# Kernel optimization log

Measured on AMD Instinct MI355X. Metric: run time of the kernel, lower is better.

The kernel has to match this reference:

```python
import jax, jax.numpy as jnp
import numpy as np

N = 2048   # graph nodes
K = 3      # Chebyshev order of LSTM cell graph conv
IN = 2     # input feature dim (in/out flow)
H = 64     # hidden dim
B = 16     # batch
T = 12     # encoder sequence length


def _cheb(L, x, order):
    """Chebyshev polynomial features. x: [B, N, F] -> [B, N, order*F]."""
    Tk = [x]
    if order > 1:
        Tk.append(jnp.einsum('nm,bmf->bnf', L, x))
    for _ in range(2, order):
        Tk.append(2.0 * jnp.einsum('nm,bmf->bnf', L, Tk[-1]) - Tk[-2])
    return jnp.concatenate(Tk, axis=-1)


def _cell(L, x, h, c, W, b):
    """Graph-conv LSTM cell. x: [B,N,IN], h/c: [B,N,H]."""
    comb = jnp.concatenate([x, h], axis=-1)          # [B, N, IN+H]
    gates = _cheb(L, comb, K) @ W + b                # [B, N, 4H]
    i, f, o, g = jnp.split(gates, 4, axis=-1)
    c2 = jax.nn.sigmoid(f) * c + jax.nn.sigmoid(i) * jnp.tanh(g)
    h2 = jax.nn.sigmoid(o) * jnp.tanh(c2)
    return h2, c2


def setup_inputs() -> dict:
    rng = np.random.default_rng(0)
    # random sparse symmetric adjacency (avg degree ~8) -> normalized Laplacian
    A = rng.random((N, N)) < 8.0 / N
    A = np.triu(A, 1)
    A = (A | A.T).astype(np.float32)
    d = np.clip(A.sum(1), 1.0, None)
    dinv = 1.0 / np.sqrt(d)
    Lap = (np.eye(N, dtype=np.float32) - dinv[:, None] * A * dinv[None, :]).astype(np.float32)

    key = jax.random.key(0)
    k1, k2, k3 = jax.random.split(key, 3)
    return {
        'input_tensor': jax.random.normal(k1, (B, T, N, IN), jnp.float32),
        'L': jnp.asarray(Lap),
        'W_cell': jax.random.normal(k2, (K * (IN + H), 4 * H), jnp.float32) * 0.05,
        'b_cell': jnp.zeros((4 * H,), jnp.float32),
        'W0': jax.random.normal(k3, (H, IN), jnp.float32) * 0.05,
        'b0': jnp.zeros((IN,), jnp.float32),
        'future': 12,
    }


def reference(input_tensor, L, W_cell, b_cell, W0, b0, future):
    bsz = input_tensor.shape[0]
    h0 = jnp.zeros((bsz, N, H), input_tensor.dtype)
    c0 = jnp.zeros((bsz, N, H), input_tensor.dtype)

    # encoder: unroll ConvLSTM over the input sequence
    def enc_step(carry, xt):
        h, c = carry
        h, c = _cell(L, xt, h, c, W_cell, b_cell)
        return (h, c), None

    (h, c), _ = jax.lax.scan(enc_step, (h0, c0), jnp.swapaxes(input_tensor, 0, 1))

    # conv0 has K=1 => per-node linear; first prediction from last hidden state
    x = jnp.tanh(h @ W0 + b0)                         # [B, N, IN]

    def dec_step(carry, _):
        h, c, x = carry
        h, c = _cell(L, x, h, c, W_cell, b_cell)
        x2 = jnp.tanh(h @ W0 + b0)
        return (h, c, x2), x2

    _, xs = jax.lax.scan(dec_step, (h, c, x), None, length=future - 1)
    if future > 1:
        out = jnp.concatenate([x[:, None], jnp.swapaxes(xs, 0, 1)], axis=1)
    else:
        out = x[:, None]
    return out  # [B, future, N, IN]
```

## Files before the change

### kernel.cpp

```cpp
#include <hip/hip_runtime.h>
#include <cstdint>
#include <cstddef>

#define NN   2048
#define BB   16
#define TT   12
#define FUT  12
#define HH   64
#define GG   256
#define KP   224
#define ELLW 72
#define ASTR 232

typedef __attribute__((ext_vector_type(8))) short bf16x8;
typedef __attribute__((ext_vector_type(4))) float f32x4;

__device__ __forceinline__ float sigmoidf_(float x) {
    return 1.f / (1.f + __expf(-x));
}
__device__ __forceinline__ float tanhf_(float x) {
    const float e = __expf(2.f * x);
    return 1.f - 2.f / (e + 1.f);
}
__device__ __forceinline__ unsigned short f2bf(float x) {
    unsigned u = __builtin_bit_cast(unsigned, x);
    u += 0x7fffu + ((u >> 16) & 1u);
    return (unsigned short)(u >> 16);
}
__device__ __forceinline__ float bf2f(unsigned short s) {
    unsigned u = ((unsigned)s) << 16;
    return __builtin_bit_cast(float, u);
}

__global__ __launch_bounds__(256) void build_ell(
    const float* __restrict__ L, int* __restrict__ cols,
    float* __restrict__ vals, int* __restrict__ cnt)
{
    const int n = blockIdx.x;
    const int t = threadIdx.x;
    const float* row = L + (size_t)n * NN;
    float v[8];
    int c = 0;
#pragma unroll
    for (int i = 0; i < 8; ++i) {
        v[i] = row[t * 8 + i];
        c += (v[i] != 0.f);
    }
    __shared__ int s[256];
    s[t] = c;
    __syncthreads();
    for (int d = 1; d < 256; d <<= 1) {
        int add = (t >= d) ? s[t - d] : 0;
        __syncthreads();
        s[t] += add;
        __syncthreads();
    }
    int o = s[t] - c;
#pragma unroll
    for (int i = 0; i < 8; ++i) {
        if (v[i] != 0.f) {
            if (o < ELLW) {
                cols[n * ELLW + o] = t * 8 + i;
                vals[n * ELLW + o] = v[i];
            }
            ++o;
        }
    }
    if (t == 255) {
        int cn = (s[255] < ELLW) ? s[255] : ELLW;
        int cn4 = (cn + 3) & ~3;
        if (cn4 > ELLW) cn4 = ELLW;
        for (int p = cn; p < cn4; ++p) {
            cols[n * ELLW + p] = n;
            vals[n * ELLW + p] = 0.f;
        }
        cnt[n] = cn4;
    }
}

__global__ __launch_bounds__(256) void wt_prep(
    const float* __restrict__ W, short* __restrict__ Wh, short* __restrict__ Wl)
{
    const int col = blockIdx.x;
    const int k = threadIdx.x;
    if (k < KP) {
        const float x = (k < 198) ? W[(size_t)k * GG + col] : 0.f;
        const unsigned short h = f2bf(x);
        const unsigned short l = f2bf(x - bf2f(h));
        Wh[(size_t)col * KP + k] = (short)h;
        Wl[(size_t)col * KP + k] = (short)l;
    }
}

__global__ __launch_bounds__(256) void x_trans(
    const float* __restrict__ input, float* __restrict__ xt)
{
    const int o = blockIdx.x * 256 + threadIdx.x;
    const int e = o & 1;
    const int b = (o >> 1) & 15;
    const int n = (o >> 5) & (NN - 1);
    const int t = o >> 16;
    xt[o] = input[(((size_t)b * TT + t) * NN + n) * 2 + e];
}

__global__ __launch_bounds__(256) void spmm_t1(
    const float* __restrict__ xt,
    const float* __restrict__ h,
    const int* __restrict__ cols, const float* __restrict__ vals,
    const int* __restrict__ cnt,
    float* __restrict__ t1h, float* __restrict__ t1x)
{
    const int w = threadIdx.x >> 6, lane = threadIdx.x & 63;
    const int b = lane >> 2, j = lane & 3;
    const int n = blockIdx.x;
    const int cn = cnt[n];
    const int* cp = cols + n * ELLW;
    const float* vp = vals + n * ELLW;
    const int qoff = (4 * w + j) * 4;
    float a0 = 0.f, a1 = 0.f, a2 = 0.f, a3 = 0.f;
    float ax0 = 0.f, ax1 = 0.f;
#pragma unroll 4
    for (int jj = 0; jj < cn; ++jj) {
        const int m = cp[jj];
        const float v = vp[jj];
        const float4 g = *(const float4*)&h[((size_t)m * 16 + b) * HH + qoff];
        a0 += v * g.x; a1 += v * g.y; a2 += v * g.z; a3 += v * g.w;
        if (w == 0) {
            const float2 xg = *(const float2*)&xt[((size_t)m * 16 + b) * 2];
            ax0 += v * xg.x; ax1 += v * xg.y;
        }
    }
    *(float4*)&t1h[((size_t)n * 16 + b) * HH + qoff] = (float4){a0, a1, a2, a3};
    if (w == 0 && j == 0) {
        t1x[((size_t)n * 16 + b) * 2]     = ax0;
        t1x[((size_t)n * 16 + b) * 2 + 1] = ax1;
    }
}

__global__ __launch_bounds__(256, 4) void cell_fused(
    const float* __restrict__ xt,
    float* __restrict__ h, float* __restrict__ c,
    const float* __restrict__ t1h,
    const float* __restrict__ t1x,
    const int* __restrict__ cols, const float* __restrict__ vals,
    const int* __restrict__ cnt,
    const short* __restrict__ Wh, const short* __restrict__ Wl,
    const float* __restrict__ bc,
    const float* __restrict__ W0, const float* __restrict__ b0,
    float* __restrict__ xout,
    float* __restrict__ out, int jslot)
{
    __shared__ unsigned short Ah[32][ASTR];
    __shared__ unsigned short Al[32][ASTR];
    __shared__ float proj[4][32][2];
    const int tid = threadIdx.x, w = tid >> 6, lane = tid & 63;
    const int q = lane >> 4, c16 = lane & 15;
    const int b = lane >> 2, j = lane & 3;
    const int n0 = blockIdx.x * 2;
    const int qoff = (4 * w + j) * 4;

    auto put = [&](int r, int k, float v) {
        const unsigned short hi = f2bf(v);
        Ah[r][k] = hi;
        Al[r][k] = f2bf(v - bf2f(hi));
    };

    {
        const int zr = tid >> 3, zs = tid & 7;
#pragma unroll
        for (int k0 = 198; k0 < 232; k0 += 8) {
            const int k = k0 + zs;
            if (k < 232) { Ah[zr][k] = 0; Al[zr][k] = 0; }
        }
    }

#pragma unroll
    for (int ln = 0; ln < 2; ++ln) {
        const int n = n0 + ln;
        const size_t rb = (size_t)n * 16 + b;
        const int r = ln * 16 + b;
        const float4 hq = *(const float4*)&h[rb * HH + qoff];
        const float4 tq = *(const float4*)&t1h[rb * HH + qoff];
        float xo0 = 0.f, xo1 = 0.f, t160 = 0.f, t161 = 0.f;
        if (w == 1) {
            const float2 xv = *(const float2*)&xt[rb * 2];
            xo0 = xv.x; xo1 = xv.y;
            const float2 tv = *(const float2*)&t1x[rb * 2];
            t160 = tv.x; t161 = tv.y;
        }
        const int cn = cnt[n];
        const int* cp = cols + n * ELLW;
        const float* vp = vals + n * ELLW;
        float a0 = 0.f, a1 = 0.f, a2 = 0.f, a3 = 0.f, ax0 = 0.f, ax1 = 0.f;
#pragma unroll 4
        for (int jj = 0; jj < cn; ++jj) {
            const int m = cp[jj];
            const float v = vp[jj];
            const size_t mb = (size_t)m * 16 + b;
            const float4 g = *(const float4*)&t1h[mb * HH + qoff];
            a0 += v * g.x; a1 += v * g.y; a2 += v * g.z; a3 += v * g.w;
            if (w == 1) {
                const float2 gx = *(const float2*)&t1x[mb * 2];
                ax0 += v * gx.x; ax1 += v * gx.y;
            }
        }
        put(r, 2 + qoff + 0, hq.x);  put(r, 2 + qoff + 1, hq.y);
        put(r, 2 + qoff + 2, hq.z);  put(r, 2 + qoff + 3, hq.w);
        put(r, 68 + qoff + 0, tq.x); put(r, 68 + qoff + 1, tq.y);
        put(r, 68 + qoff + 2, tq.z); put(r, 68 + qoff + 3, tq.w);
        put(r, 134 + qoff + 0, 2.f * a0 - hq.x);
        put(r, 134 + qoff + 1, 2.f * a1 - hq.y);
        put(r, 134 + qoff + 2, 2.f * a2 - hq.z);
        put(r, 134 + qoff + 3, 2.f * a3 - hq.w);
        if (w == 1 && j == 0) {
            put(r, 0, xo0);   put(r, 1, xo1);
            put(r, 66, t160); put(r, 67, t161);
            put(r, 132, 2.f * ax0 - xo0);
            put(r, 133, 2.f * ax1 - xo1);
        }
    }
    __syncthreads();

    f32x4 acc[2][4];
#pragma unroll
    for (int rt = 0; rt < 2; ++rt)
#pragma unroll
        for (int g = 0; g < 4; ++g) acc[rt][g] = (f32x4){0.f, 0.f, 0.f, 0.f};

    for (int kc = 0; kc < 7; ++kc) {
        const int ko = kc * 32 + q * 8;
        bf16x8 ah[2], al[2];
#pragma unroll
        for (int rt = 0; rt < 2; ++rt) {
            ah[rt] = *(const bf16x8*)&Ah[rt * 16 + c16][ko];
            al[rt] = *(const bf16x8*)&Al[rt * 16 + c16][ko];
        }
        bf16x8 bh[4], bl[4];
#pragma unroll
        for (int g = 0; g < 4; ++g) {
            const int col = (w + 4 * g) * 16 + c16;
            const size_t wo = (size_t)col * KP + ko;
            bh[g] = *(const bf16x8*)(Wh + wo);
            bl[g] = *(const bf16x8*)(Wl + wo);
        }
#pragma unroll
        for (int rt = 0; rt < 2; ++rt)
#pragma unroll
            for (int g = 0; g < 4; ++g) {
                acc[rt][g] = __builtin_amdgcn_mfma_f32_16x16x32_bf16(ah[rt], bh[g], acc[rt][g], 0, 0, 0);
                acc[rt][g] = __builtin_amdgcn_mfma_f32_16x16x32_bf16(al[rt], bh[g], acc[rt][g], 0, 0, 0);
                acc[rt][g] = __builtin_amdgcn_mfma_f32_16x16x32_bf16(ah[rt], bl[g], acc[rt][g], 0, 0, 0);
            }
    }

    const int u = 16 * w + c16;
    const float bi = bc[u], bfv = bc[64 + u], bo = bc[128 + u], bg = bc[192 + u];
    float h2v[2][4];
#pragma unroll
    for (int rt = 0; rt < 2; ++rt) {
        const int n = n0 + rt;
#pragma unroll
        for (int reg = 0; reg < 4; ++reg) {
            const int bb = q * 4 + reg;
            const size_t idx = ((size_t)n * 16 + bb) * HH + u;
            const float ig = sigmoidf_(acc[rt][0][reg] + bi);
            const float fg = sigmoidf_(acc[rt][1][reg] + bfv);
            const float og = sigmoidf_(acc[rt][2][reg] + bo);
            const float gg = tanhf_(acc[rt][3][reg] + bg);
            const float c2 = fg * c[idx] + ig * gg;
            const float h2 = og * tanhf_(c2);
            c[idx] = c2;
            h[idx] = h2;
            h2v[rt][reg] = h2;
        }
    }

    if (jslot >= 0) {
        const float w0u = W0[u * 2], w1u = W0[u * 2 + 1];
#pragma unroll
        for (int rt = 0; rt < 2; ++rt) {
#pragma unroll
            for (int reg = 0; reg < 4; ++reg) {
                float s0 = h2v[rt][reg] * w0u;
                float s1 = h2v[rt][reg] * w1u;
#pragma unroll
                for (int d = 1; d <= 8; d <<= 1) {
                    s0 += __shfl_xor(s0, d, 64);
                    s1 += __shfl_xor(s1, d, 64);
                }
                if (c16 == 0) {
                    const int lr = rt * 16 + q * 4 + reg;
                    proj[w][lr][0] = s0;
                    proj[w][lr][1] = s1;
                }
            }
        }
        __syncthreads();
        if (tid < 64) {
            const int lr = tid >> 1, comp = tid & 1;
            const float v = proj[0][lr][comp] + proj[1][lr][comp] +
                            proj[2][lr][comp] + proj[3][lr][comp] + b0[comp];
            const float y = tanhf_(v);
            const int n = n0 + (lr >> 4);
            const int bb = lr & 15;
            xout[((size_t)n * 16 + bb) * 2 + comp] = y;
            out[(((size_t)bb * FUT + jslot) * NN + n) * 2 + comp] = y;
        }
    }
}

extern "C" void kernel_launch(void* const* d_in, const int* in_sizes, int n_in,
                              void* d_out, int out_size, void* d_ws, size_t ws_size,
                              hipStream_t stream)
{
    const float* input = (const float*)d_in[0];
    const float* L     = (const float*)d_in[1];
    const float* W     = (const float*)d_in[2];
    const float* bc    = (const float*)d_in[3];
    const float* W0    = (const float*)d_in[4];
    const float* b0    = (const float*)d_in[5];

    char* ws = (char*)d_ws;
    size_t off = 0;
    auto carve = [&](size_t bytes) {
        void* p = ws + off;
        off += (bytes + 255) & ~(size_t)255;
        return p;
    };
    int*   cols  = (int*)  carve((size_t)NN * ELLW * 4);
    float* vals  = (float*)carve((size_t)NN * ELLW * 4);
    int*   cnt   = (int*)  carve((size_t)NN * 4);
    float* t1h   = (float*)carve((size_t)NN * 16 * HH * 4);
    float* t1x   = (float*)carve((size_t)NN * 16 * 2 * 4);
    float* h     = (float*)carve((size_t)NN * 16 * HH * 4);
    float* c     = (float*)carve((size_t)NN * 16 * HH * 4);
    float* xbuf  = (float*)carve((size_t)NN * 16 * 2 * 4);
    float* xtall = (float*)carve((size_t)TT * NN * 16 * 2 * 4);
    short* Wh    = (short*)carve((size_t)GG * KP * 2);
    short* Wl    = (short*)carve((size_t)GG * KP * 2);
    float* out   = (float*)d_out;

    build_ell<<<NN, 256, 0, stream>>>(L, cols, vals, cnt);
    wt_prep<<<GG, 256, 0, stream>>>(W, Wh, Wl);
    x_trans<<<(TT * NN * 16 * 2) / 256, 256, 0, stream>>>(input, xtall);
    hipMemsetAsync(h, 0, (size_t)NN * 16 * HH * 4, stream);
    hipMemsetAsync(c, 0, (size_t)NN * 16 * HH * 4, stream);

    for (int t = 0; t < TT; ++t) {
        const float* xt = xtall + (size_t)t * NN * 16 * 2;
        spmm_t1<<<NN, 256, 0, stream>>>(xt, h, cols, vals, cnt, t1h, t1x);
        cell_fused<<<NN / 2, 256, 0, stream>>>(xt, h, c, t1h, t1x, cols, vals, cnt,
                                               Wh, Wl, bc, W0, b0, xbuf, out,
                                               (t == TT - 1) ? 0 : -1);
    }
    for (int jstep = 1; jstep < FUT; ++jstep) {
        spmm_t1<<<NN, 256, 0, stream>>>(xbuf, h, cols, vals, cnt, t1h, t1x);
        cell_fused<<<NN / 2, 256, 0, stream>>>(xbuf, h, c, t1h, t1x, cols, vals, cnt,
                                               Wh, Wl, bc, W0, b0, xbuf, out, jstep);
    }
}
```

Measured before the change: 1.176 ms.

## Split second Chebyshev SpMM out of fused cell kernel into separate kernel

Moves the T2 = 2*L*T1 - T0 sparse product out of the GEMM/LSTM kernel into a new spmm_t2 kernel launched with one block per node, so the fused cell kernel only stages precomputed features. Both SpMM kernels now use a 4-wide unrolled inner loop over a count rounded up to a multiple of four, with every unused ELL slot padded with zero weights, and request higher occupancy through launch bounds. This aims to give the gather-heavy SpMM full parallelism instead of sharing blocks with the MFMA kernel. In exchange it adds an extra launch per step and extra global traffic to write and read the T2 buffers.

```diff
diff --git a/kernel.cpp b/kernel.cpp
--- a/kernel.cpp
+++ b/kernel.cpp
@@ -66,16 +66,12 @@
             ++o;
         }
     }
-    if (t == 255) {
-        int cn = (s[255] < ELLW) ? s[255] : ELLW;
-        int cn4 = (cn + 3) & ~3;
-        if (cn4 > ELLW) cn4 = ELLW;
-        for (int p = cn; p < cn4; ++p) {
-            cols[n * ELLW + p] = n;
-            vals[n * ELLW + p] = 0.f;
-        }
-        cnt[n] = cn4;
-    }
+    const int cn = (s[255] < ELLW) ? s[255] : ELLW;
+    for (int p = cn + t; p < ELLW; p += 256) {
+        cols[n * ELLW + p] = n;
+        vals[n * ELLW + p] = 0.f;
+    }
+    if (t == 255) cnt[n] = cn;
 }
 
 __global__ __launch_bounds__(256) void wt_prep(
@@ -103,7 +99,7 @@
     xt[o] = input[(((size_t)b * TT + t) * NN + n) * 2 + e];
 }
 
-__global__ __launch_bounds__(256) void spmm_t1(
+__global__ __launch_bounds__(256, 8) void spmm_t1(
     const float* __restrict__ xt,
     const float* __restrict__ h,
     const int* __restrict__ cols, const float* __restrict__ vals,
@@ -113,21 +109,25 @@
     const int w = threadIdx.x >> 6, lane = threadIdx.x & 63;
     const int b = lane >> 2, j = lane & 3;
     const int n = blockIdx.x;
-    const int cn = cnt[n];
+    const int cn4 = (cnt[n] + 3) & ~3;
     const int* cp = cols + n * ELLW;
     const float* vp = vals + n * ELLW;
     const int qoff = (4 * w + j) * 4;
     float a0 = 0.f, a1 = 0.f, a2 = 0.f, a3 = 0.f;
     float ax0 = 0.f, ax1 = 0.f;
-#pragma unroll 4
-    for (int jj = 0; jj < cn; ++jj) {
-        const int m = cp[jj];
-        const float v = vp[jj];
-        const float4 g = *(const float4*)&h[((size_t)m * 16 + b) * HH + qoff];
-        a0 += v * g.x; a1 += v * g.y; a2 += v * g.z; a3 += v * g.w;
-        if (w == 0) {
-            const float2 xg = *(const float2*)&xt[((size_t)m * 16 + b) * 2];
-            ax0 += v * xg.x; ax1 += v * xg.y;
+#pragma unroll 2
+    for (int jj = 0; jj < cn4; jj += 4) {
+#pragma unroll
+        for (int u = 0; u < 4; ++u) {
+            const int m = cp[jj + u];
+            const float v = vp[jj + u];
+            const size_t mb = (size_t)m * 16 + b;
+            const float4 g = *(const float4*)&h[mb * HH + qoff];
+            a0 += v * g.x; a1 += v * g.y; a2 += v * g.z; a3 += v * g.w;
+            if (w == 0) {
+                const float2 xg = *(const float2*)&xt[mb * 2];
+                ax0 += v * xg.x; ax1 += v * xg.y;
+            }
         }
     }
     *(float4*)&t1h[((size_t)n * 16 + b) * HH + qoff] = (float4){a0, a1, a2, a3};
@@ -137,13 +137,55 @@
     }
 }
 
-__global__ __launch_bounds__(256, 4) void cell_fused(
+__global__ __launch_bounds__(256, 8) void spmm_t2(
     const float* __restrict__ xt,
-    float* __restrict__ h, float* __restrict__ c,
+    const float* __restrict__ h,
     const float* __restrict__ t1h,
     const float* __restrict__ t1x,
     const int* __restrict__ cols, const float* __restrict__ vals,
     const int* __restrict__ cnt,
+    float* __restrict__ t2h, float* __restrict__ t2x)
+{
+    const int w = threadIdx.x >> 6, lane = threadIdx.x & 63;
+    const int b = lane >> 2, j = lane & 3;
+    const int n = blockIdx.x;
+    const int cn4 = (cnt[n] + 3) & ~3;
+    const int* cp = cols + n * ELLW;
+    const float* vp = vals + n * ELLW;
+    const int qoff = (4 * w + j) * 4;
+    float a0 = 0.f, a1 = 0.f, a2 = 0.f, a3 = 0.f;
+    float ax0 = 0.f, ax1 = 0.f;
+#pragma unroll 2
+    for (int jj = 0; jj < cn4; jj += 4) {
+#pragma unroll
+        for (int u = 0; u < 4; ++u) {
+            const int m = cp[jj + u];
+            const float v = vp[jj + u];
+            const size_t mb = (size_t)m * 16 + b;
+            const float4 g = *(const float4*)&t1h[mb * HH + qoff];
+            a0 += v * g.x; a1 += v * g.y; a2 += v * g.z; a3 += v * g.w;
+            if (w == 0) {
+                const float2 gx = *(const float2*)&t1x[mb * 2];
+                ax0 += v * gx.x; ax1 += v * gx.y;
+            }
+        }
+    }
+    const size_t rb = (size_t)n * 16 + b;
+    const float4 hq = *(const float4*)&h[rb * HH + qoff];
+    *(float4*)&t2h[rb * HH + qoff] =
+        (float4){2.f * a0 - hq.x, 2.f * a1 - hq.y, 2.f * a2 - hq.z, 2.f * a3 - hq.w};
+    if (w == 0 && j == 0) {
+        const float2 xv = *(const float2*)&xt[rb * 2];
+        t2x[rb * 2]     = 2.f * ax0 - xv.x;
+        t2x[rb * 2 + 1] = 2.f * ax1 - xv.y;
+    }
+}
+
+__global__ __launch_bounds__(256, 4) void cell_fused(
+    const float* __restrict__ xt,
+    float* __restrict__ h, float* __restrict__ c,
+    const float* __restrict__ t1h, const float* __restrict__ t1x,
+    const float* __restrict__ t2h, const float* __restrict__ t2x,
     const short* __restrict__ Wh, const short* __restrict__ Wl,
     const float* __restrict__ bc,
     const float* __restrict__ W0, const float* __restrict__ b0,
@@ -181,42 +223,20 @@
         const int r = ln * 16 + b;
         const float4 hq = *(const float4*)&h[rb * HH + qoff];
         const float4 tq = *(const float4*)&t1h[rb * HH + qoff];
-        float xo0 = 0.f, xo1 = 0.f, t160 = 0.f, t161 = 0.f;
-        if (w == 1) {
+        const float4 zq = *(const float4*)&t2h[rb * HH + qoff];
+        put(r, 2 + qoff + 0, hq.x);   put(r, 2 + qoff + 1, hq.y);
+        put(r, 2 + qoff + 2, hq.z);   put(r, 2 + qoff + 3, hq.w);
+        put(r, 68 + qoff + 0, tq.x);  put(r, 68 + qoff + 1, tq.y);
+        put(r, 68 + qoff + 2, tq.z);  put(r, 68 + qoff + 3, tq.w);
+        put(r, 134 + qoff + 0, zq.x); put(r, 134 + qoff + 1, zq.y);
+        put(r, 134 + qoff + 2, zq.z); put(r, 134 + qoff + 3, zq.w);
+        if (w == 1 && j == 0) {
             const float2 xv = *(const float2*)&xt[rb * 2];
-            xo0 = xv.x; xo1 = xv.y;
             const float2 tv = *(const float2*)&t1x[rb * 2];
-            t160 = tv.x; t161 = tv.y;
-        }
-        const int cn = cnt[n];
-        const int* cp = cols + n * ELLW;
-        const float* vp = vals + n * ELLW;
-        float a0 = 0.f, a1 = 0.f, a2 = 0.f, a3 = 0.f, ax0 = 0.f, ax1 = 0.f;
-#pragma unroll 4
-        for (int jj = 0; jj < cn; ++jj) {
-            const int m = cp[jj];
-            const float v = vp[jj];
-            const size_t mb = (size_t)m * 16 + b;
-            const float4 g = *(const float4*)&t1h[mb * HH + qoff];
-            a0 += v * g.x; a1 += v * g.y; a2 += v * g.z; a3 += v * g.w;
-            if (w == 1) {
-                const float2 gx = *(const float2*)&t1x[mb * 2];
-                ax0 += v * gx.x; ax1 += v * gx.y;
-            }
-        }
-        put(r, 2 + qoff + 0, hq.x);  put(r, 2 + qoff + 1, hq.y);
-        put(r, 2 + qoff + 2, hq.z);  put(r, 2 + qoff + 3, hq.w);
-        put(r, 68 + qoff + 0, tq.x); put(r, 68 + qoff + 1, tq.y);
-        put(r, 68 + qoff + 2, tq.z); put(r, 68 + qoff + 3, tq.w);
-        put(r, 134 + qoff + 0, 2.f * a0 - hq.x);
-        put(r, 134 + qoff + 1, 2.f * a1 - hq.y);
-        put(r, 134 + qoff + 2, 2.f * a2 - hq.z);
-        put(r, 134 + qoff + 3, 2.f * a3 - hq.w);
-        if (w == 1 && j == 0) {
-            put(r, 0, xo0);   put(r, 1, xo1);
-            put(r, 66, t160); put(r, 67, t161);
-            put(r, 132, 2.f * ax0 - xo0);
-            put(r, 133, 2.f * ax1 - xo1);
+            const float2 zv = *(const float2*)&t2x[rb * 2];
+            put(r, 0, xv.x);   put(r, 1, xv.y);
+            put(r, 66, tv.x);  put(r, 67, tv.y);
+            put(r, 132, zv.x); put(r, 133, zv.y);
         }
     }
     __syncthreads();
@@ -332,6 +352,8 @@
     int*   cnt   = (int*)  carve((size_t)NN * 4);
     float* t1h   = (float*)carve((size_t)NN * 16 * HH * 4);
     float* t1x   = (float*)carve((size_t)NN * 16 * 2 * 4);
+    float* t2h   = (float*)carve((size_t)NN * 16 * HH * 4);
+    float* t2x   = (float*)carve((size_t)NN * 16 * 2 * 4);
     float* h     = (float*)carve((size_t)NN * 16 * HH * 4);
     float* c     = (float*)carve((size_t)NN * 16 * HH * 4);
     float* xbuf  = (float*)carve((size_t)NN * 16 * 2 * 4);
@@ -349,13 +371,15 @@
     for (int t = 0; t < TT; ++t) {
         const float* xt = xtall + (size_t)t * NN * 16 * 2;
         spmm_t1<<<NN, 256, 0, stream>>>(xt, h, cols, vals, cnt, t1h, t1x);
-        cell_fused<<<NN / 2, 256, 0, stream>>>(xt, h, c, t1h, t1x, cols, vals, cnt,
+        spmm_t2<<<NN, 256, 0, stream>>>(xt, h, t1h, t1x, cols, vals, cnt, t2h, t2x);
+        cell_fused<<<NN / 2, 256, 0, stream>>>(xt, h, c, t1h, t1x, t2h, t2x,
                                                Wh, Wl, bc, W0, b0, xbuf, out,
                                                (t == TT - 1) ? 0 : -1);
     }
     for (int jstep = 1; jstep < FUT; ++jstep) {
         spmm_t1<<<NN, 256, 0, stream>>>(xbuf, h, cols, vals, cnt, t1h, t1x);
-        cell_fused<<<NN / 2, 256, 0, stream>>>(xbuf, h, c, t1h, t1x, cols, vals, cnt,
+        spmm_t2<<<NN, 256, 0, stream>>>(xbuf, h, t1h, t1x, cols, vals, cnt, t2h, t2x);
+        cell_fused<<<NN / 2, 256, 0, stream>>>(xbuf, h, c, t1h, t1x, t2h, t2x,
                                                Wh, Wl, bc, W0, b0, xbuf, out, jstep);
     }
 }
```

Result: slower. 1.334 ms (+13.4%).

## Slab state by batch pair and remap SpMM blocks for cache locality

Applied to the files above, without the earlier changes.

Reorganizes the h, c, t1 and x buffers into 8 slabs, each holding two batch elements, laid out [p][n][bb][feature]. Each block now handles one slab across several nodes, so neighbor gathers in the SpMM touch a smaller working set that fits better in cache. The ELL width shrinks from 72 to 32, with padding done in parallel and loops unrolled by groups of four. The risk is that nodes with degree above 32 are truncated, which would silently drop Laplacian entries.

```diff
diff --git a/kernel.cpp b/kernel.cpp
--- a/kernel.cpp
+++ b/kernel.cpp
@@ -9,7 +9,7 @@
 #define HH   64
 #define GG   256
 #define KP   224
-#define ELLW 72
+#define ELLW 32
 #define ASTR 232
 
 typedef __attribute__((ext_vector_type(8))) short bf16x8;
@@ -30,6 +30,13 @@
 __device__ __forceinline__ float bf2f(unsigned short s) {
     unsigned u = ((unsigned)s) << 16;
     return __builtin_bit_cast(float, u);
+}
+
+__device__ __forceinline__ size_t idxH(int p, int n, int bb) {
+    return ((((size_t)p * NN + n) << 1) + bb) << 6;
+}
+__device__ __forceinline__ size_t idxX(int p, int n, int bb) {
+    return ((((size_t)p * NN + n) << 1) + bb) << 1;
 }
 
 __global__ __launch_bounds__(256) void build_ell(
@@ -66,16 +73,12 @@
             ++o;
         }
     }
-    if (t == 255) {
-        int cn = (s[255] < ELLW) ? s[255] : ELLW;
-        int cn4 = (cn + 3) & ~3;
-        if (cn4 > ELLW) cn4 = ELLW;
-        for (int p = cn; p < cn4; ++p) {
-            cols[n * ELLW + p] = n;
-            vals[n * ELLW + p] = 0.f;
-        }
-        cnt[n] = cn4;
-    }
+    const int cn = (s[255] < ELLW) ? s[255] : ELLW;
+    for (int pp = cn + t; pp < ELLW; pp += 256) {
+        cols[n * ELLW + pp] = n;
+        vals[n * ELLW + pp] = 0.f;
+    }
+    if (t == 255) cnt[n] = cn;
 }
 
 __global__ __launch_bounds__(256) void wt_prep(
@@ -97,67 +100,74 @@
 {
     const int o = blockIdx.x * 256 + threadIdx.x;
     const int e = o & 1;
-    const int b = (o >> 1) & 15;
-    const int n = (o >> 5) & (NN - 1);
+    const int bb = (o >> 1) & 1;
+    const int n = (o >> 2) & (NN - 1);
+    const int p = (o >> 13) & 7;
     const int t = o >> 16;
+    const int b = p * 2 + bb;
     xt[o] = input[(((size_t)b * TT + t) * NN + n) * 2 + e];
 }
 
-__global__ __launch_bounds__(256) void spmm_t1(
+__global__ __launch_bounds__(256, 8) void spmm_t1(
     const float* __restrict__ xt,
-    const float* __restrict__ h,
+    const float* __restrict__ hs,
     const int* __restrict__ cols, const float* __restrict__ vals,
     const int* __restrict__ cnt,
-    float* __restrict__ t1h, float* __restrict__ t1x)
-{
-    const int w = threadIdx.x >> 6, lane = threadIdx.x & 63;
-    const int b = lane >> 2, j = lane & 3;
-    const int n = blockIdx.x;
-    const int cn = cnt[n];
+    float* __restrict__ t1s, float* __restrict__ t1xs)
+{
+    const int bid = blockIdx.x;
+    const int p = bid & 7, g = bid >> 3;
+    const int t = threadIdx.x;
+    const int row = t >> 4, q = t & 15;
+    const int n = g * 8 + (row >> 1), bb = row & 1;
+    const int cn4 = (cnt[n] + 3) & ~3;
     const int* cp = cols + n * ELLW;
     const float* vp = vals + n * ELLW;
-    const int qoff = (4 * w + j) * 4;
+    const size_t slabH = (size_t)p * NN * 2 * 64;
     float a0 = 0.f, a1 = 0.f, a2 = 0.f, a3 = 0.f;
     float ax0 = 0.f, ax1 = 0.f;
-#pragma unroll 4
-    for (int jj = 0; jj < cn; ++jj) {
-        const int m = cp[jj];
-        const float v = vp[jj];
-        const float4 g = *(const float4*)&h[((size_t)m * 16 + b) * HH + qoff];
-        a0 += v * g.x; a1 += v * g.y; a2 += v * g.z; a3 += v * g.w;
-        if (w == 0) {
-            const float2 xg = *(const float2*)&xt[((size_t)m * 16 + b) * 2];
-            ax0 += v * xg.x; ax1 += v * xg.y;
-        }
-    }
-    *(float4*)&t1h[((size_t)n * 16 + b) * HH + qoff] = (float4){a0, a1, a2, a3};
-    if (w == 0 && j == 0) {
-        t1x[((size_t)n * 16 + b) * 2]     = ax0;
-        t1x[((size_t)n * 16 + b) * 2 + 1] = ax1;
+#pragma unroll 2
+    for (int jj = 0; jj < cn4; jj += 4) {
+#pragma unroll
+        for (int u = 0; u < 4; ++u) {
+            const int m = cp[jj + u];
+            const float v = vp[jj + u];
+            const float4 gq = *(const float4*)&hs[idxH(p, m, bb) + 4 * q];
+            a0 += v * gq.x; a1 += v * gq.y; a2 += v * gq.z; a3 += v * gq.w;
+            if (q == 0) {
+                const float2 xg = *(const float2*)&xt[idxX(p, m, bb)];
+                ax0 += v * xg.x; ax1 += v * xg.y;
+            }
+        }
+    }
+    *(float4*)&t1s[idxH(p, n, bb) + 4 * q] = (float4){a0, a1, a2, a3};
+    if (q == 0) {
+        t1xs[idxX(p, n, bb)]     = ax0;
+        t1xs[idxX(p, n, bb) + 1] = ax1;
     }
 }
 
 __global__ __launch_bounds__(256, 4) void cell_fused(
     const float* __restrict__ xt,
-    float* __restrict__ h, float* __restrict__ c,
-    const float* __restrict__ t1h,
-    const float* __restrict__ t1x,
+    float* __restrict__ hs, float* __restrict__ cs,
+    const float* __restrict__ t1s,
+    const float* __restrict__ t1xs,
     const int* __restrict__ cols, const float* __restrict__ vals,
     const int* __restrict__ cnt,
     const short* __restrict__ Wh, const short* __restrict__ Wl,
     const float* __restrict__ bc,
     const float* __restrict__ W0, const float* __restrict__ b0,
-    float* __restrict__ xout,
+    float* __restrict__ xouts,
     float* __restrict__ out, int jslot)
 {
     __shared__ unsigned short Ah[32][ASTR];
     __shared__ unsigned short Al[32][ASTR];
     __shared__ float proj[4][32][2];
     const int tid = threadIdx.x, w = tid >> 6, lane = tid & 63;
-    const int q = lane >> 4, c16 = lane & 15;
-    const int b = lane >> 2, j = lane & 3;
-    const int n0 = blockIdx.x * 2;
-    const int qoff = (4 * w + j) * 4;
+    const int qw = lane >> 4, c16 = lane & 15;
+    const int bid = blockIdx.x;
+    const int p = bid & 7, g = bid >> 3;
+    const int n0 = g * 16;
 
     auto put = [&](int r, int k, float v) {
         const unsigned short hi = f2bf(v);
@@ -175,44 +185,48 @@
     }
 
 #pragma unroll
-    for (int ln = 0; ln < 2; ++ln) {
-        const int n = n0 + ln;
-        const size_t rb = (size_t)n * 16 + b;
-        const int r = ln * 16 + b;
-        const float4 hq = *(const float4*)&h[rb * HH + qoff];
-        const float4 tq = *(const float4*)&t1h[rb * HH + qoff];
+    for (int half = 0; half < 2; ++half) {
+        const int r = (tid >> 4) + half * 16;
+        const int q = tid & 15;
+        const int n = n0 + (r >> 1), bb = r & 1;
+        const size_t rbase = idxH(p, n, bb);
+        const float4 hq = *(const float4*)&hs[rbase + 4 * q];
+        const float4 tq = *(const float4*)&t1s[rbase + 4 * q];
         float xo0 = 0.f, xo1 = 0.f, t160 = 0.f, t161 = 0.f;
-        if (w == 1) {
-            const float2 xv = *(const float2*)&xt[rb * 2];
+        if (q == 0) {
+            const float2 xv = *(const float2*)&xt[idxX(p, n, bb)];
             xo0 = xv.x; xo1 = xv.y;
-            const float2 tv = *(const float2*)&t1x[rb * 2];
+            const float2 tv = *(const float2*)&t1xs[idxX(p, n, bb)];
             t160 = tv.x; t161 = tv.y;
         }
-        const int cn = cnt[n];
+        const int cn4 = (cnt[n] + 3) & ~3;
         const int* cp = cols + n * ELLW;
         const float* vp = vals + n * ELLW;
         float a0 = 0.f, a1 = 0.f, a2 = 0.f, a3 = 0.f, ax0 = 0.f, ax1 = 0.f;
-#pragma unroll 4
-        for (int jj = 0; jj < cn; ++jj) {
-            const int m = cp[jj];
-            const float v = vp[jj];
-            const size_t mb = (size_t)m * 16 + b;
-            const float4 g = *(const float4*)&t1h[mb * HH + qoff];
-            a0 += v * g.x; a1 += v * g.y; a2 += v * g.z; a3 += v * g.w;
-            if (w == 1) {
-                const float2 gx = *(const float2*)&t1x[mb * 2];
-                ax0 += v * gx.x; ax1 += v * gx.y;
-            }
-        }
-        put(r, 2 + qoff + 0, hq.x);  put(r, 2 + qoff + 1, hq.y);
-        put(r, 2 + qoff + 2, hq.z);  put(r, 2 + qoff + 3, hq.w);
-        put(r, 68 + qoff + 0, tq.x); put(r, 68 + qoff + 1, tq.y);
-        put(r, 68 + qoff + 2, tq.z); put(r, 68 + qoff + 3, tq.w);
-        put(r, 134 + qoff + 0, 2.f * a0 - hq.x);
-        put(r, 134 + qoff + 1, 2.f * a1 - hq.y);
-        put(r, 134 + qoff + 2, 2.f * a2 - hq.z);
-        put(r, 134 + qoff + 3, 2.f * a3 - hq.w);
-        if (w == 1 && j == 0) {
+#pragma unroll 2
+        for (int jj = 0; jj < cn4; jj += 4) {
+#pragma unroll
+            for (int u = 0; u < 4; ++u) {
+                const int m = cp[jj + u];
+                const float v = vp[jj + u];
+                const float4 gq = *(const float4*)&t1s[idxH(p, m, bb) + 4 * q];
+                a0 += v * gq.x; a1 += v * gq.y; a2 += v * gq.z; a3 += v * gq.w;
+                if (q == 0) {
+                    const float2 gx = *(const float2*)&t1xs[idxX(p, m, bb)];
+                    ax0 += v * gx.x; ax1 += v * gx.y;
+                }
+            }
+        }
+        const int ko = 4 * q;
+        put(r, 2 + ko + 0, hq.x);  put(r, 2 + ko + 1, hq.y);
+        put(r, 2 + ko + 2, hq.z);  put(r, 2 + ko + 3, hq.w);
+        put(r, 68 + ko + 0, tq.x); put(r, 68 + ko + 1, tq.y);
+        put(r, 68 + ko + 2, tq.z); put(r, 68 + ko + 3, tq.w);
+        put(r, 134 + ko + 0, 2.f * a0 - hq.x);
+        put(r, 134 + ko + 1, 2.f * a1 - hq.y);
+        put(r, 134 + ko + 2, 2.f * a2 - hq.z);
+        put(r, 134 + ko + 3, 2.f * a3 - hq.w);
+        if (q == 0) {
             put(r, 0, xo0);   put(r, 1, xo1);
             put(r, 66, t160); put(r, 67, t161);
             put(r, 132, 2.f * ax0 - xo0);
@@ -225,10 +239,10 @@
 #pragma unroll
     for (int rt = 0; rt < 2; ++rt)
 #pragma unroll
-        for (int g = 0; g < 4; ++g) acc[rt][g] = (f32x4){0.f, 0.f, 0.f, 0.f};
+        for (int gg2 = 0; gg2 < 4; ++gg2) acc[rt][gg2] = (f32x4){0.f, 0.f, 0.f, 0.f};
 
     for (int kc = 0; kc < 7; ++kc) {
-        const int ko = kc * 32 + q * 8;
+        const int ko = kc * 32 + qw * 8;
         bf16x8 ah[2], al[2];
 #pragma unroll
         for (int rt = 0; rt < 2; ++rt) {
@@ -237,40 +251,40 @@
         }
         bf16x8 bh[4], bl[4];
 #pragma unroll
-        for (int g = 0; g < 4; ++g) {
-            const int col = (w + 4 * g) * 16 + c16;
+        for (int gg2 = 0; gg2 < 4; ++gg2) {
+            const int col = (w + 4 * gg2) * 16 + c16;
             const size_t wo = (size_t)col * KP + ko;
-            bh[g] = *(const bf16x8*)(Wh + wo);
-            bl[g] = *(const bf16x8*)(Wl + wo);
+            bh[gg2] = *(const bf16x8*)(Wh + wo);
+            bl[gg2] = *(const bf16x8*)(Wl + wo);
         }
 #pragma unroll
         for (int rt = 0; rt < 2; ++rt)
 #pragma unroll
-            for (int g = 0; g < 4; ++g) {
-                acc[rt][g] = __builtin_amdgcn_mfma_f32_16x16x32_bf16(ah[rt], bh[g], acc[rt][g], 0, 0, 0);
-                acc[rt][g] = __builtin_amdgcn_mfma_f32_16x16x32_bf16(al[rt], bh[g], acc[rt][g], 0, 0, 0);
-                acc[rt][g] = __builtin_amdgcn_mfma_f32_16x16x32_bf16(ah[rt], bl[g], acc[rt][g], 0, 0, 0);
+            for (int gg2 = 0; gg2 < 4; ++gg2) {
+                acc[rt][gg2] = __builtin_amdgcn_mfma_f32_16x16x32_bf16(ah[rt], bh[gg2], acc[rt][gg2], 0, 0, 0);
+                acc[rt][gg2] = __builtin_amdgcn_mfma_f32_16x16x32_bf16(al[rt], bh[gg2], acc[rt][gg2], 0, 0, 0);
+                acc[rt][gg2] = __builtin_amdgcn_mfma_f32_16x16x32_bf16(ah[rt], bl[gg2], acc[rt][gg2], 0, 0, 0);
             }
     }
 
     const int u = 16 * w + c16;
     const float bi = bc[u], bfv = bc[64 + u], bo = bc[128 + u], bg = bc[192 + u];
+    const size_t blk = ((size_t)p * NN + n0) * 2 * 64;
     float h2v[2][4];
 #pragma unroll
     for (int rt = 0; rt < 2; ++rt) {
-        const int n = n0 + rt;
 #pragma unroll
         for (int reg = 0; reg < 4; ++reg) {
-            const int bb = q * 4 + reg;
-            const size_t idx = ((size_t)n * 16 + bb) * HH + u;
+            const int row = rt * 16 + qw * 4 + reg;
+            const size_t idx = blk + (size_t)row * 64 + u;
             const float ig = sigmoidf_(acc[rt][0][reg] + bi);
             const float fg = sigmoidf_(acc[rt][1][reg] + bfv);
             const float og = sigmoidf_(acc[rt][2][reg] + bo);
-            const float gg = tanhf_(acc[rt][3][reg] + bg);
-            const float c2 = fg * c[idx] + ig * gg;
+            const float gg2 = tanhf_(acc[rt][3][reg] + bg);
+            const float c2 = fg * cs[idx] + ig * gg2;
             const float h2 = og * tanhf_(c2);
-            c[idx] = c2;
-            h[idx] = h2;
+            cs[idx] = c2;
+            hs[idx] = h2;
             h2v[rt][reg] = h2;
         }
     }
@@ -289,7 +303,7 @@
                     s1 += __shfl_xor(s1, d, 64);
                 }
                 if (c16 == 0) {
-                    const int lr = rt * 16 + q * 4 + reg;
+                    const int lr = rt * 16 + qw * 4 + reg;
                     proj[w][lr][0] = s0;
                     proj[w][lr][1] = s1;
                 }
@@ -301,10 +315,10 @@
             const float v = proj[0][lr][comp] + proj[1][lr][comp] +
                             proj[2][lr][comp] + proj[3][lr][comp] + b0[comp];
             const float y = tanhf_(v);
-            const int n = n0 + (lr >> 4);
-            const int bb = lr & 15;
-            xout[((size_t)n * 16 + bb) * 2 + comp] = y;
-            out[(((size_t)bb * FUT + jslot) * NN + n) * 2 + comp] = y;
+            const int n = n0 + (lr >> 1), bb = lr & 1;
+            const int b = p * 2 + bb;
+            xouts[idxX(p, n, bb) + comp] = y;
+            out[(((size_t)b * FUT + jslot) * NN + n) * 2 + comp] = y;
         }
     }
 }
@@ -330,10 +344,10 @@
     int*   cols  = (int*)  carve((size_t)NN * ELLW * 4);
     float* vals  = (float*)carve((size_t)NN * ELLW * 4);
     int*   cnt   = (int*)  carve((size_t)NN * 4);
-    float* t1h   = (float*)carve((size_t)NN * 16 * HH * 4);
-    float* t1x   = (float*)carve((size_t)NN * 16 * 2 * 4);
-    float* h     = (float*)carve((size_t)NN * 16 * HH * 4);
-    float* c     = (float*)carve((size_t)NN * 16 * HH * 4);
+    float* t1s   = (float*)carve((size_t)NN * 16 * HH * 4);
+    float* t1xs  = (float*)carve((size_t)NN * 16 * 2 * 4);
+    float* hs    = (float*)carve((size_t)NN * 16 * HH * 4);
+    float* cs    = (float*)carve((size_t)NN * 16 * HH * 4);
     float* xbuf  = (float*)carve((size_t)NN * 16 * 2 * 4);
     float* xtall = (float*)carve((size_t)TT * NN * 16 * 2 * 4);
     short* Wh    = (short*)carve((size_t)GG * KP * 2);
@@ -343,19 +357,19 @@
     build_ell<<<NN, 256, 0, stream>>>(L, cols, vals, cnt);
     wt_prep<<<GG, 256, 0, stream>>>(W, Wh, Wl);
     x_trans<<<(TT * NN * 16 * 2) / 256, 256, 0, stream>>>(input, xtall);
-    hipMemsetAsync(h, 0, (size_t)NN * 16 * HH * 4, stream);
-    hipMemsetAsync(c, 0, (size_t)NN * 16 * HH * 4, stream);
+    hipMemsetAsync(hs, 0, (size_t)NN * 16 * HH * 4, stream);
+    hipMemsetAsync(cs, 0, (size_t)NN * 16 * HH * 4, stream);
 
     for (int t = 0; t < TT; ++t) {
         const float* xt = xtall + (size_t)t * NN * 16 * 2;
-        spmm_t1<<<NN, 256, 0, stream>>>(xt, h, cols, vals, cnt, t1h, t1x);
-        cell_fused<<<NN / 2, 256, 0, stream>>>(xt, h, c, t1h, t1x, cols, vals, cnt,
+        spmm_t1<<<NN, 256, 0, stream>>>(xt, hs, cols, vals, cnt, t1s, t1xs);
+        cell_fused<<<NN / 2, 256, 0, stream>>>(xt, hs, cs, t1s, t1xs, cols, vals, cnt,
                                                Wh, Wl, bc, W0, b0, xbuf, out,
                                                (t == TT - 1) ? 0 : -1);
     }
     for (int jstep = 1; jstep < FUT; ++jstep) {
-        spmm_t1<<<NN, 256, 0, stream>>>(xbuf, h, cols, vals, cnt, t1h, t1x);
-        cell_fused<<<NN / 2, 256, 0, stream>>>(xbuf, h, c, t1h, t1x, cols, vals, cnt,
+        spmm_t1<<<NN, 256, 0, stream>>>(xbuf, hs, cols, vals, cnt, t1s, t1xs);
+        cell_fused<<<NN / 2, 256, 0, stream>>>(xbuf, hs, cs, t1s, t1xs, cols, vals, cnt,
                                                Wh, Wl, bc, W0, b0, xbuf, out, jstep);
     }
 }
```

Result: slower. 1.393 ms (+18.5%).
